# Performance work log

Hardware: AMD Instinct MI355X
Metric: run time of the kernel (lower is better)

## Reference

```python
import jax, jax.numpy as jnp
import numpy as np

H = 11          # hidden size
L = 5           # num layers
G = 4 * H       # gates (i,f,g,o) per PyTorch order


def run_dir(x, Wih, Whh, b, reverse):
    """Single-direction LSTM over x [B,T,D] -> [B,T,H]."""
    pre = jnp.einsum('btd,gd->btg', x, Wih) + b      # [B,T,4H] input projections
    pre = pre.transpose(1, 0, 2)                     # [T,B,4H]
    if reverse:
        pre = pre[::-1]
    B = x.shape[0]
    h0 = jnp.zeros((B, H), x.dtype)
    c0 = jnp.zeros((B, H), x.dtype)

    def step(carry, gt):
        h, c = carry
        g = gt + h @ Whh.T                           # [B,4H]
        i, f, gg, o = jnp.split(g, 4, axis=-1)
        i = jax.nn.sigmoid(i)
        f = jax.nn.sigmoid(f)
        gg = jnp.tanh(gg)
        o = jax.nn.sigmoid(o)
        c = f * c + i * gg
        h = o * jnp.tanh(c)
        return (h, c), h

    _, hs = jax.lax.scan(step, (h0, c0), pre)        # hs [T,B,H]
    if reverse:
        hs = hs[::-1]
    return hs.transpose(1, 0, 2)                     # [B,T,H]


def setup_inputs() -> dict:
    key = jax.random.key(0)
    ks = jax.random.split(key, 6)
    x = jax.random.normal(ks[0], (2048, 1, 32, 512), dtype=jnp.float32)
    # PyTorch LSTM params: layer0 input=1; layers1-4 input=2H (bidir concat)
    W_ih0 = jax.random.normal(ks[1], (2, G, 1), dtype=jnp.float32) * 0.2
    W_ih_rest = jax.random.normal(ks[2], (L - 1, 2, G, 2 * H), dtype=jnp.float32) * 0.1
    W_hh = jax.random.normal(ks[3], (L, 2, G, H), dtype=jnp.float32) * 0.1
    b_ih = jax.random.normal(ks[4], (L, 2, G), dtype=jnp.float32) * 0.05
    b_hh = jax.random.normal(ks[5], (L, 2, G), dtype=jnp.float32) * 0.05
    return {"x": x, "W_ih0": W_ih0, "W_ih_rest": W_ih_rest, "W_hh": W_hh,
            "b_ih": b_ih, "b_hh": b_hh}


def reference(x, W_ih0, W_ih_rest, W_hh, b_ih, b_hh):
    # x: [B, C=1, height, width] -> sum over height -> [B, C, W] -> [B, W, C]
    inp = x.sum(2).transpose(0, 2, 1)                # [B, W, 1]
    for l in range(L):
        outs = []
        for d in range(2):                           # 0=fwd, 1=bwd
            Wih = W_ih0[d] if l == 0 else W_ih_rest[l - 1, d]
            b = b_ih[l, d] + b_hh[l, d]
            outs.append(run_dir(inp, Wih, W_hh[l, d], b, reverse=(d == 1)))
        inp = jnp.concatenate(outs, axis=-1)         # [B, W, 2H]
    return inp
```

## Files before the change

### kernel.cpp

```cpp
#include <hip/hip_runtime.h>

constexpr int TT = 512;
constexpr int BB = 2048;
constexpr int HH = 11;
constexpr int GG = 44;
constexpr int NL = 5;

typedef float v2f __attribute__((ext_vector_type(2)));
typedef float v4f __attribute__((ext_vector_type(4)));

__device__ __forceinline__ float dpp_q0(float v) {
    return __int_as_float(__builtin_amdgcn_mov_dpp(__float_as_int(v), 0x00, 0xF, 0xF, false));
}
__device__ __forceinline__ float dpp_q1(float v) {
    return __int_as_float(__builtin_amdgcn_mov_dpp(__float_as_int(v), 0x55, 0xF, 0xF, false));
}
__device__ __forceinline__ float dpp_q3(float v) {
    return __int_as_float(__builtin_amdgcn_mov_dpp(__float_as_int(v), 0xFF, 0xF, 0xF, false));
}
__device__ __forceinline__ float dpp_qswap2(float v) {
    return __int_as_float(__builtin_amdgcn_mov_dpp(__float_as_int(v), 0x4E, 0xF, 0xF, false));
}

__global__ void reduce_x(const float* __restrict__ x, float* __restrict__ inp) {
    int t = blockIdx.x * 256 + threadIdx.x;
    int b = blockIdx.y;
    const float* p = x + (size_t)b * 32 * TT + t;
    float s = 0.f;
#pragma unroll
    for (int k = 0; k < 32; k++) s += p[k * TT];
    inp[(size_t)b * TT + t] = s;
}

template <int IND>
__global__ __launch_bounds__(256, 4)
void lstm_layer(
    const float* __restrict__ xin,
    float* __restrict__ out,
    const float* __restrict__ Wih,
    const float* __restrict__ Whh,
    const float* __restrict__ bih,
    const float* __restrict__ bhh)
{
    constexpr int NP    = (IND > 1) ? IND / 2 : 1;
    constexpr int CH    = (IND == 1) ? 64 : 32;
    constexpr int NCH   = TT / CH;
    constexpr int NLD   = (CH * IND) / 64;
    constexpr int RS    = (IND == 1) ? 1 : 24;
    constexpr int BUFSZ = CH * RS;

    __shared__ __align__(16) float smem[4 * 2 * BUFSZ];

    const float L2E   = 1.4426950408889634f;
    const float NL2E  = -L2E;
    const float N2L2E = -2.f * L2E;

    int tid  = threadIdx.x;
    int lane = tid & 63;
    int wid  = tid >> 6;
    int u = lane >> 2;
    int q = lane & 3;
    bool active = (u < HH);
    int grow = q * HH + u;

    int seq = __builtin_amdgcn_readfirstlane((int)blockIdx.x * 4 + wid);
    int b = seq >> 1;
    int d = seq & 1;

    float esc    = (q == 2) ? N2L2E : NL2E;
    float ascale = (q == 2) ? 2.f * N2L2E : 1.f;
    float aoff   = (q == 2) ? -N2L2E : 0.f;

    v2f   wih2[NP];
    float wih0 = 0.f;
    v2f   whh2[6];
    v2f   bias2;
    if (active) {
        const float* wi = Wih + (size_t)(d * GG + grow) * IND;
        if constexpr (IND == 1) {
            wih0 = wi[0] * esc;
        } else {
#pragma unroll
            for (int p = 0; p < NP; p++) wih2[p] = ((const v2f*)wi)[p] * esc;
        }
        const float* wh = Whh + (size_t)(d * GG + grow) * HH;
#pragma unroll
        for (int k = 0; k < 5; k++)
            whh2[k] = (v2f){wh[2 * k] * esc, wh[2 * k + 1] * esc};
        whh2[5] = (v2f){wh[10] * esc, 0.f};
        float bv = (bih[d * GG + grow] + bhh[d * GG + grow]) * esc;
        bias2 = (v2f){bv, 0.f};
    } else {
        if constexpr (IND != 1) {
#pragma unroll
            for (int p = 0; p < NP; p++) wih2[p] = (v2f){0.f, 0.f};
        }
#pragma unroll
        for (int k = 0; k < 6; k++) whh2[k] = (v2f){0.f, 0.f};
        bias2 = (v2f){0.f, 0.f};
    }

    float hprev = 0.f;
    float c = 0.f;

    const int ostep = d ? -22 : 22;
    float* op = out + (size_t)b * TT * 22 + (size_t)(d ? (TT - 1) * 22 : 0)
                    + d * HH + u;
    const bool doStore = (q == 0) && active;

    float* xls = smem + wid * (2 * BUFSZ);

    const float* gbase = xin + (size_t)b * TT * IND
                             + (size_t)(d ? (TT - CH) * IND : 0);
    const int gstep = d ? -(CH * IND) : (CH * IND);

    int wdw[NLD];
#pragma unroll
    for (int k = 0; k < NLD; k++) {
        int p = k * 64 + lane;
        int row = p / IND;
        int col = p - row * IND;
        int r2 = d ? (CH - 1 - row) : row;
        wdw[k] = r2 * RS + col;
    }

    {
        float p0[NLD];
#pragma unroll
        for (int k = 0; k < NLD; k++) p0[k] = gbase[k * 64 + lane];
#pragma unroll
        for (int k = 0; k < NLD; k++) xls[wdw[k]] = p0[k];
    }
    int buf = 0;
    const float* lrow = xls;
    const float* gnext = gbase + gstep;

    v2f   xA[NP], xB[NP];
    float xAs = 0.f, xBs = 0.f;

#define LOAD_ROW(DST, PTR)                                                    \
    do {                                                                      \
        if constexpr (IND == 1) {                                             \
            DST##s = (PTR)[0];                                                \
        } else {                                                              \
            _Pragma("unroll")                                                 \
            for (int i4 = 0; i4 < 5; i4++) {                                  \
                v4f t4 = ((const v4f*)(PTR))[i4];                             \
                DST[2 * i4]     = (v2f){t4.x, t4.y};                          \
                DST[2 * i4 + 1] = (v2f){t4.z, t4.w};                          \
            }                                                                 \
            DST[10] = ((const v2f*)(PTR))[10];                                \
        }                                                                     \
    } while (0)

    LOAD_ROW(xA, lrow);

#define LSTM_STEP(XC, XN, DOPF)                                               \
    do {                                                                      \
        v2f accA, accB;                                                       \
        if constexpr (IND == 1) {                                             \
            accA = bias2;                                                     \
            accB = (v2f){0.f, 0.f};                                           \
        } else {                                                              \
            accA = __builtin_elementwise_fma(XC[0], wih2[0], bias2);          \
            accB = XC[1] * wih2[1];                                           \
            _Pragma("unroll")                                                 \
            for (int p = 2; p < NP; p++) {                                    \
                if (p & 1) accB = __builtin_elementwise_fma(XC[p], wih2[p], accB);\
                else       accA = __builtin_elementwise_fma(XC[p], wih2[p], accA);\
            }                                                                 \
        }                                                                     \
        if (DOPF) { lrow += RS; LOAD_ROW(XN, lrow); }                         \
            \
        asm volatile(                                                         \
            "v_readlane_b32 s20, %2, 0\n\t"                                   \
            "v_readlane_b32 s21, %2, 4\n\t"                                   \
            "v_readlane_b32 s22, %2, 8\n\t"                                   \
            "v_readlane_b32 s23, %2, 12\n\t"                                  \
            "v_readlane_b32 s24, %2, 16\n\t"                                  \
            "v_readlane_b32 s25, %2, 20\n\t"                                  \
            "v_readlane_b32 s26, %2, 24\n\t"                                  \
            "v_readlane_b32 s27, %2, 28\n\t"                                  \
            "v_readlane_b32 s28, %2, 32\n\t"                                  \
            "v_readlane_b32 s29, %2, 36\n\t"                                  \
            "v_readlane_b32 s30, %2, 40\n\t"                                  \
            "v_readlane_b32 s31, %2, 44\n\t"                                  \
            "v_pk_fma_f32 %0, s[20:21], %3, %0\n\t"                           \
            "v_pk_fma_f32 %1, s[22:23], %4, %1\n\t"                           \
            "v_pk_fma_f32 %0, s[24:25], %5, %0\n\t"                           \
            "v_pk_fma_f32 %1, s[26:27], %6, %1\n\t"                           \
            "v_pk_fma_f32 %0, s[28:29], %7, %0\n\t"                           \
            "v_pk_fma_f32 %1, s[30:31], %8, %1"                               \
            : "+v"(accA), "+v"(accB)                                          \
            : "v"(hprev), "v"(whh2[0]), "v"(whh2[1]), "v"(whh2[2]),           \
              "v"(whh2[3]), "v"(whh2[4]), "v"(whh2[5])                        \
            : "s20","s21","s22","s23","s24","s25","s26","s27",                \
              "s28","s29","s30","s31");                                       \
        v2f s2 = accA + accB;                                                 \
        float pre = s2.x + s2.y;                                              \
        if constexpr (IND == 1) pre = fmaf(XC##s, wih0, pre);                 \
        float e   = __builtin_amdgcn_exp2f(pre);                              \
        float act = fmaf(ascale, __builtin_amdgcn_rcpf(1.f + e), aoff);       \
        float ig  = act * dpp_qswap2(act);                  \
        float igb = dpp_q0(ig);                                               \
        float fv  = dpp_q1(act);                                              \
        float ov  = dpp_q3(act);                                              \
        c = fmaf(fv, c, igb);                                                 \
        float e2 = __builtin_amdgcn_exp2f(c);                                 \
        float th = fmaf(2.f, __builtin_amdgcn_rcpf(1.f + e2), -1.f);          \
        float h  = ov * th;                                 \
        if (doStore) *op = h;                                                 \
        op += ostep;                                                          \
        hprev = h;                                                            \
    } while (0)

    for (int ch = 0; ch < NCH; ch++) {
        const bool last = (ch + 1 == NCH);
        float pf[NLD];
        if (!last) {
#pragma unroll
            for (int k = 0; k < NLD; k++) pf[k] = gnext[k * 64 + lane];
        }
        for (int sl = 0; sl < CH - 2; sl += 2) {
            LSTM_STEP(xA, xB, true);
            LSTM_STEP(xB, xA, true);
        }
        LSTM_STEP(xA, xB, true);
        LSTM_STEP(xB, xA, false);
        if (!last) {
            float* swn = xls + ((buf ^ 1) ? BUFSZ : 0);
#pragma unroll
            for (int k = 0; k < NLD; k++) swn[wdw[k]] = pf[k];
            buf ^= 1;
            lrow = swn;
            LOAD_ROW(xA, lrow);
            gnext += gstep;
        }
    }
#undef LSTM_STEP
#undef LOAD_ROW
}

extern "C" void kernel_launch(void* const* d_in, const int* in_sizes, int n_in,
                              void* d_out, int out_size, void* d_ws, size_t ws_size,
                              hipStream_t stream) {
    const float* x        = (const float*)d_in[0];
    const float* W_ih0    = (const float*)d_in[1];
    const float* W_ih_rest= (const float*)d_in[2];
    const float* W_hh     = (const float*)d_in[3];
    const float* b_ih     = (const float*)d_in[4];
    const float* b_hh     = (const float*)d_in[5];
    float* out = (float*)d_out;

    const size_t perB = (size_t)TT * 22 * sizeof(float);
    int chunk = BB;
    while (chunk > 2 && (size_t)chunk * perB > ws_size) chunk >>= 1;
    float* wsbuf = (float*)d_ws;

    for (int c0 = 0; c0 < BB; c0 += chunk) {
        const float* xc   = x + (size_t)c0 * 32 * TT;
        float*       outc = out + (size_t)c0 * TT * 22;
        const int nblk = (chunk * 2) / 4;

        reduce_x<<<dim3(2, chunk), 256, 0, stream>>>(xc, wsbuf);

        lstm_layer<1><<<nblk, 256, 0, stream>>>(wsbuf, outc, W_ih0, W_hh, b_ih, b_hh);

        for (int l = 1; l < NL; l++) {
            const float* src = (l & 1) ? outc : wsbuf;
            float*       dst = (l & 1) ? wsbuf : outc;
            lstm_layer<22><<<nblk, 256, 0, stream>>>(
                src, dst,
                W_ih_rest + (size_t)(l - 1) * 2 * GG * 22,
                W_hh + (size_t)l * 2 * GG * HH,
                b_ih + (size_t)l * 2 * GG,
                b_hh + (size_t)l * 2 * GG);
        }
    }
}
```

Measured before the change: 1.230 ms.

## Run forward and backward LSTM directions interleaved in one wavefront

Each wavefront now handles one batch element and runs both directions together, alternating the two independent recurrences step by step. The goal is to hide the latency of the serial dependency chain (readlane, pk_fma, exp, rcp, dpp) by giving the scheduler two independent chains, and to halve the wave count. In exchange it needs more registers (launch bounds lowered to 2 blocks per SM), uses twice the LDS per wave with an unpadded row stride, and has half as many waves resident to hide latency.

```diff
diff --git a/kernel.cpp b/kernel.cpp
--- a/kernel.cpp
+++ b/kernel.cpp
@@ -7,7 +7,6 @@
 constexpr int NL = 5;
 
 typedef float v2f __attribute__((ext_vector_type(2)));
-typedef float v4f __attribute__((ext_vector_type(4)));
 
 __device__ __forceinline__ float dpp_q0(float v) {
     return __int_as_float(__builtin_amdgcn_mov_dpp(__float_as_int(v), 0x00, 0xF, 0xF, false));
@@ -33,7 +32,7 @@
 }
 
 template <int IND>
-__global__ __launch_bounds__(256, 4)
+__global__ __launch_bounds__(256, 2)
 void lstm_layer(
     const float* __restrict__ xin,
     float* __restrict__ out,
@@ -46,10 +45,9 @@
     constexpr int CH    = (IND == 1) ? 64 : 32;
     constexpr int NCH   = TT / CH;
     constexpr int NLD   = (CH * IND) / 64;
-    constexpr int RS    = (IND == 1) ? 1 : 24;
-    constexpr int BUFSZ = CH * RS;
-
-    __shared__ __align__(16) float smem[4 * 2 * BUFSZ];
+    constexpr int BUFSZ = CH * IND;
+
+    __shared__ float smem[4 * 4 * BUFSZ];
 
     const float L2E   = 1.4426950408889634f;
     const float NL2E  = -L2E;
@@ -63,80 +61,96 @@
     bool active = (u < HH);
     int grow = q * HH + u;
 
-    int seq = __builtin_amdgcn_readfirstlane((int)blockIdx.x * 4 + wid);
-    int b = seq >> 1;
-    int d = seq & 1;
+    int b = __builtin_amdgcn_readfirstlane((int)blockIdx.x * 4 + wid);
 
     float esc    = (q == 2) ? N2L2E : NL2E;
     float ascale = (q == 2) ? 2.f * N2L2E : 1.f;
     float aoff   = (q == 2) ? -N2L2E : 0.f;
 
-    v2f   wih2[NP];
-    float wih0 = 0.f;
-    v2f   whh2[6];
-    v2f   bias2;
+    v2f   wihA[NP], wihB[NP];
+    float wihA0 = 0.f, wihB0 = 0.f;
+    v2f   whhA[6], whhB[6];
+    v2f   biasA, biasB;
     if (active) {
-        const float* wi = Wih + (size_t)(d * GG + grow) * IND;
+        const float* wiA = Wih + (size_t)grow * IND;
+        const float* wiB = Wih + (size_t)(GG + grow) * IND;
         if constexpr (IND == 1) {
-            wih0 = wi[0] * esc;
+            wihA0 = wiA[0] * esc;
+            wihB0 = wiB[0] * esc;
         } else {
 #pragma unroll
-            for (int p = 0; p < NP; p++) wih2[p] = ((const v2f*)wi)[p] * esc;
-        }
-        const float* wh = Whh + (size_t)(d * GG + grow) * HH;
-#pragma unroll
-        for (int k = 0; k < 5; k++)
-            whh2[k] = (v2f){wh[2 * k] * esc, wh[2 * k + 1] * esc};
-        whh2[5] = (v2f){wh[10] * esc, 0.f};
-        float bv = (bih[d * GG + grow] + bhh[d * GG + grow]) * esc;
-        bias2 = (v2f){bv, 0.f};
+            for (int p = 0; p < NP; p++) wihA[p] = ((const v2f*)wiA)[p] * esc;
+#pragma unroll
+            for (int p = 0; p < NP; p++) wihB[p] = ((const v2f*)wiB)[p] * esc;
+        }
+        const float* whA = Whh + (size_t)grow * HH;
+        const float* whB = Whh + (size_t)(GG + grow) * HH;
+#pragma unroll
+        for (int k = 0; k < 5; k++) {
+            whhA[k] = (v2f){whA[2 * k] * esc, whA[2 * k + 1] * esc};
+            whhB[k] = (v2f){whB[2 * k] * esc, whB[2 * k + 1] * esc};
+        }
+        whhA[5] = (v2f){whA[10] * esc, 0.f};
+        whhB[5] = (v2f){whB[10] * esc, 0.f};
+        biasA = (v2f){(bih[grow] + bhh[grow]) * esc, 0.f};
+        biasB = (v2f){(bih[GG + grow] + bhh[GG + grow]) * esc, 0.f};
     } else {
         if constexpr (IND != 1) {
 #pragma unroll
-            for (int p = 0; p < NP; p++) wih2[p] = (v2f){0.f, 0.f};
-        }
-#pragma unroll
-        for (int k = 0; k < 6; k++) whh2[k] = (v2f){0.f, 0.f};
-        bias2 = (v2f){0.f, 0.f};
-    }
-
-    float hprev = 0.f;
-    float c = 0.f;
-
-    const int ostep = d ? -22 : 22;
-    float* op = out + (size_t)b * TT * 22 + (size_t)(d ? (TT - 1) * 22 : 0)
-                    + d * HH + u;
+            for (int p = 0; p < NP; p++) { wihA[p] = (v2f){0.f, 0.f}; wihB[p] = (v2f){0.f, 0.f}; }
+        }
+#pragma unroll
+        for (int k = 0; k < 6; k++) { whhA[k] = (v2f){0.f, 0.f}; whhB[k] = (v2f){0.f, 0.f}; }
+        biasA = (v2f){0.f, 0.f};
+        biasB = (v2f){0.f, 0.f};
+    }
+
+    float hA = 0.f, hB = 0.f;
+    float cA = 0.f, cB = 0.f;
+
+    float* opA = out + (size_t)b * TT * 22 + u;
+    float* opB = out + (size_t)b * TT * 22 + (size_t)(TT - 1) * 22 + HH + u;
     const bool doStore = (q == 0) && active;
 
-    float* xls = smem + wid * (2 * BUFSZ);
-
-    const float* gbase = xin + (size_t)b * TT * IND
-                             + (size_t)(d ? (TT - CH) * IND : 0);
-    const int gstep = d ? -(CH * IND) : (CH * IND);
-
-    int wdw[NLD];
+    float* base = smem + wid * (4 * BUFSZ);
+    float* xa0 = base;
+    float* xa1 = base + BUFSZ;
+    float* xb0 = base + 2 * BUFSZ;
+    float* xb1 = base + 3 * BUFSZ;
+
+    const float* gA = xin + (size_t)b * TT * IND;
+    const float* gB = xin + (size_t)b * TT * IND + (size_t)(TT - CH) * IND;
+    const int gstep = CH * IND;
+
+    int wdwB[NLD];
 #pragma unroll
     for (int k = 0; k < NLD; k++) {
         int p = k * 64 + lane;
         int row = p / IND;
         int col = p - row * IND;
-        int r2 = d ? (CH - 1 - row) : row;
-        wdw[k] = r2 * RS + col;
+        wdwB[k] = (CH - 1 - row) * IND + col;
     }
 
     {
-        float p0[NLD];
-#pragma unroll
-        for (int k = 0; k < NLD; k++) p0[k] = gbase[k * 64 + lane];
-#pragma unroll
-        for (int k = 0; k < NLD; k++) xls[wdw[k]] = p0[k];
-    }
-    int buf = 0;
-    const float* lrow = xls;
-    const float* gnext = gbase + gstep;
-
-    v2f   xA[NP], xB[NP];
-    float xAs = 0.f, xBs = 0.f;
+        float pA[NLD], pB[NLD];
+#pragma unroll
+        for (int k = 0; k < NLD; k++) pA[k] = gA[k * 64 + lane];
+#pragma unroll
+        for (int k = 0; k < NLD; k++) pB[k] = gB[k * 64 + lane];
+#pragma unroll
+        for (int k = 0; k < NLD; k++) xa0[k * 64 + lane] = pA[k];
+#pragma unroll
+        for (int k = 0; k < NLD; k++) xb0[wdwB[k]] = pB[k];
+    }
+    const float* gnA = gA + gstep;
+    const float* gnB = gB - gstep;
+    float* bufA = xa0;
+    float* bufB = xb0;
+    const float* lrA = bufA;
+    const float* lrB = bufB;
+
+    v2f   Xa0[NP], Xa1[NP], Xb0r[NP], Xb1r[NP];
+    float Xa0s = 0.f, Xa1s = 0.f, Xb0rs = 0.f, Xb1rs = 0.f;
 
 #define LOAD_ROW(DST, PTR)                                                    \
     do {                                                                      \
@@ -144,100 +158,131 @@
             DST##s = (PTR)[0];                                                \
         } else {                                                              \
             _Pragma("unroll")                                                 \
-            for (int i4 = 0; i4 < 5; i4++) {                                  \
-                v4f t4 = ((const v4f*)(PTR))[i4];                             \
-                DST[2 * i4]     = (v2f){t4.x, t4.y};                          \
-                DST[2 * i4 + 1] = (v2f){t4.z, t4.w};                          \
-            }                                                                 \
-            DST[10] = ((const v2f*)(PTR))[10];                                \
+            for (int p = 0; p < NP; p++) DST[p] = ((const v2f*)(PTR))[p];     \
         }                                                                     \
     } while (0)
 
-    LOAD_ROW(xA, lrow);
-
-#define LSTM_STEP(XC, XN, DOPF)                                               \
+    LOAD_ROW(Xa0, lrA);
+    LOAD_ROW(Xb0r, lrB);
+
+#define HDOT_ASM(A0, A1, HV, W)                                               \
+    asm volatile(                                                             \
+        "v_readlane_b32 s20, %2, 0\n\t"                                       \
+        "v_readlane_b32 s21, %2, 4\n\t"                                       \
+        "v_readlane_b32 s22, %2, 8\n\t"                                       \
+        "v_readlane_b32 s23, %2, 12\n\t"                                      \
+        "v_readlane_b32 s24, %2, 16\n\t"                                      \
+        "v_readlane_b32 s25, %2, 20\n\t"                                      \
+        "v_readlane_b32 s26, %2, 24\n\t"                                      \
+        "v_readlane_b32 s27, %2, 28\n\t"                                      \
+        "v_readlane_b32 s28, %2, 32\n\t"                                      \
+        "v_readlane_b32 s29, %2, 36\n\t"                                      \
+        "v_readlane_b32 s30, %2, 40\n\t"                                      \
+        "v_readlane_b32 s31, %2, 44\n\t"                                      \
+        "v_pk_fma_f32 %0, s[20:21], %3, %0\n\t"                               \
+        "v_pk_fma_f32 %1, s[22:23], %4, %1\n\t"                               \
+        "v_pk_fma_f32 %0, s[24:25], %5, %0\n\t"                               \
+        "v_pk_fma_f32 %1, s[26:27], %6, %1\n\t"                               \
+        "v_pk_fma_f32 %0, s[28:29], %7, %0\n\t"                               \
+        "v_pk_fma_f32 %1, s[30:31], %8, %1"                                   \
+        : "+v"(A0), "+v"(A1)                                                  \
+        : "v"(HV), "v"(W[0]), "v"(W[1]), "v"(W[2]),                           \
+          "v"(W[3]), "v"(W[4]), "v"(W[5])                                     \
+        : "s20","s21","s22","s23","s24","s25","s26","s27",                    \
+          "s28","s29","s30","s31")
+
+#define LSTM_STEP2(CA, NA, CB, NB, DOPF)                                      \
     do {                                                                      \
-        v2f accA, accB;                                                       \
+        v2f aA0, aA1, aB0, aB1;                                               \
         if constexpr (IND == 1) {                                             \
-            accA = bias2;                                                     \
-            accB = (v2f){0.f, 0.f};                                           \
+            aA0 = biasA; aA1 = (v2f){0.f, 0.f};                               \
+            aB0 = biasB; aB1 = (v2f){0.f, 0.f};                               \
         } else {                                                              \
-            accA = __builtin_elementwise_fma(XC[0], wih2[0], bias2);          \
-            accB = XC[1] * wih2[1];                                           \
+            aA0 = __builtin_elementwise_fma(CA[0], wihA[0], biasA);           \
+            aA1 = CA[1] * wihA[1];                                            \
+            aB0 = __builtin_elementwise_fma(CB[0], wihB[0], biasB);           \
+            aB1 = CB[1] * wihB[1];                                            \
             _Pragma("unroll")                                                 \
             for (int p = 2; p < NP; p++) {                                    \
-                if (p & 1) accB = __builtin_elementwise_fma(XC[p], wih2[p], accB);\
-                else       accA = __builtin_elementwise_fma(XC[p], wih2[p], accA);\
+                if (p & 1) { aA1 = __builtin_elementwise_fma(CA[p], wihA[p], aA1); \
+                             aB1 = __builtin_elementwise_fma(CB[p], wihB[p], aB1); } \
+                else       { aA0 = __builtin_elementwise_fma(CA[p], wihA[p], aA0); \
+                             aB0 = __builtin_elementwise_fma(CB[p], wihB[p], aB0); } \
             }                                                                 \
         }                                                                     \
-        if (DOPF) { lrow += RS; LOAD_ROW(XN, lrow); }                         \
-            \
-        asm volatile(                                                         \
-            "v_readlane_b32 s20, %2, 0\n\t"                                   \
-            "v_readlane_b32 s21, %2, 4\n\t"                                   \
-            "v_readlane_b32 s22, %2, 8\n\t"                                   \
-            "v_readlane_b32 s23, %2, 12\n\t"                                  \
-            "v_readlane_b32 s24, %2, 16\n\t"                                  \
-            "v_readlane_b32 s25, %2, 20\n\t"                                  \
-            "v_readlane_b32 s26, %2, 24\n\t"                                  \
-            "v_readlane_b32 s27, %2, 28\n\t"                                  \
-            "v_readlane_b32 s28, %2, 32\n\t"                                  \
-            "v_readlane_b32 s29, %2, 36\n\t"                                  \
-            "v_readlane_b32 s30, %2, 40\n\t"                                  \
-            "v_readlane_b32 s31, %2, 44\n\t"                                  \
-            "v_pk_fma_f32 %0, s[20:21], %3, %0\n\t"                           \
-            "v_pk_fma_f32 %1, s[22:23], %4, %1\n\t"                           \
-            "v_pk_fma_f32 %0, s[24:25], %5, %0\n\t"                           \
-            "v_pk_fma_f32 %1, s[26:27], %6, %1\n\t"                           \
-            "v_pk_fma_f32 %0, s[28:29], %7, %0\n\t"                           \
-            "v_pk_fma_f32 %1, s[30:31], %8, %1"                               \
-            : "+v"(accA), "+v"(accB)                                          \
-            : "v"(hprev), "v"(whh2[0]), "v"(whh2[1]), "v"(whh2[2]),           \
-              "v"(whh2[3]), "v"(whh2[4]), "v"(whh2[5])                        \
-            : "s20","s21","s22","s23","s24","s25","s26","s27",                \
-              "s28","s29","s30","s31");                                       \
-        v2f s2 = accA + accB;                                                 \
-        float pre = s2.x + s2.y;                                              \
-        if constexpr (IND == 1) pre = fmaf(XC##s, wih0, pre);                 \
-        float e   = __builtin_amdgcn_exp2f(pre);                              \
-        float act = fmaf(ascale, __builtin_amdgcn_rcpf(1.f + e), aoff);       \
-        float ig  = act * dpp_qswap2(act);                  \
-        float igb = dpp_q0(ig);                                               \
-        float fv  = dpp_q1(act);                                              \
-        float ov  = dpp_q3(act);                                              \
-        c = fmaf(fv, c, igb);                                                 \
-        float e2 = __builtin_amdgcn_exp2f(c);                                 \
-        float th = fmaf(2.f, __builtin_amdgcn_rcpf(1.f + e2), -1.f);          \
-        float h  = ov * th;                                 \
-        if (doStore) *op = h;                                                 \
-        op += ostep;                                                          \
-        hprev = h;                                                            \
+        if (DOPF) {                                                           \
+            lrA += IND; LOAD_ROW(NA, lrA);                                    \
+            lrB += IND; LOAD_ROW(NB, lrB);                                    \
+        }                                                                     \
+        HDOT_ASM(aA0, aA1, hA, whhA);                                         \
+        HDOT_ASM(aB0, aB1, hB, whhB);                                         \
+        v2f sA = aA0 + aA1;                                                   \
+        v2f sB = aB0 + aB1;                                                   \
+        float preA = sA.x + sA.y;                                             \
+        float preB = sB.x + sB.y;                                             \
+        if constexpr (IND == 1) {                                             \
+            preA = fmaf(CA##s, wihA0, preA);                                  \
+            preB = fmaf(CB##s, wihB0, preB);                                  \
+        }                                                                     \
+        float eA   = __builtin_amdgcn_exp2f(preA);                            \
+        float eB   = __builtin_amdgcn_exp2f(preB);                            \
+        float actA = fmaf(ascale, __builtin_amdgcn_rcpf(1.f + eA), aoff);     \
+        float actB = fmaf(ascale, __builtin_amdgcn_rcpf(1.f + eB), aoff);     \
+        float igA  = actA * dpp_qswap2(actA);                                 \
+        float igB  = actB * dpp_qswap2(actB);                                 \
+        float igbA = dpp_q0(igA);                                             \
+        float igbB = dpp_q0(igB);                                             \
+        float fvA  = dpp_q1(actA);                                            \
+        float fvB  = dpp_q1(actB);                                            \
+        float ovA  = dpp_q3(actA);                                            \
+        float ovB  = dpp_q3(actB);                                            \
+        cA = fmaf(fvA, cA, igbA);                                             \
+        cB = fmaf(fvB, cB, igbB);                                             \
+        float e2A = __builtin_amdgcn_exp2f(cA);                               \
+        float e2B = __builtin_amdgcn_exp2f(cB);                               \
+        float thA = fmaf(2.f, __builtin_amdgcn_rcpf(1.f + e2A), -1.f);        \
+        float thB = fmaf(2.f, __builtin_amdgcn_rcpf(1.f + e2B), -1.f);        \
+        float hA_ = ovA * thA;                                                \
+        float hB_ = ovB * thB;                                                \
+        if (doStore) { *opA = hA_; *opB = hB_; }                              \
+        opA += 22;                                                            \
+        opB -= 22;                                                            \
+        hA = hA_;                                                             \
+        hB = hB_;                                                             \
     } while (0)
 
     for (int ch = 0; ch < NCH; ch++) {
         const bool last = (ch + 1 == NCH);
-        float pf[NLD];
+        float pfA[NLD], pfB[NLD];
         if (!last) {
 #pragma unroll
-            for (int k = 0; k < NLD; k++) pf[k] = gnext[k * 64 + lane];
+            for (int k = 0; k < NLD; k++) pfA[k] = gnA[k * 64 + lane];
+#pragma unroll
+            for (int k = 0; k < NLD; k++) pfB[k] = gnB[k * 64 + lane];
         }
         for (int sl = 0; sl < CH - 2; sl += 2) {
-            LSTM_STEP(xA, xB, true);
-            LSTM_STEP(xB, xA, true);
-        }
-        LSTM_STEP(xA, xB, true);
-        LSTM_STEP(xB, xA, false);
+            LSTM_STEP2(Xa0, Xa1, Xb0r, Xb1r, true);
+            LSTM_STEP2(Xa1, Xa0, Xb1r, Xb0r, true);
+        }
+        LSTM_STEP2(Xa0, Xa1, Xb0r, Xb1r, true);
+        LSTM_STEP2(Xa1, Xa0, Xb1r, Xb0r, false);
         if (!last) {
-            float* swn = xls + ((buf ^ 1) ? BUFSZ : 0);
-#pragma unroll
-            for (int k = 0; k < NLD; k++) swn[wdw[k]] = pf[k];
-            buf ^= 1;
-            lrow = swn;
-            LOAD_ROW(xA, lrow);
-            gnext += gstep;
-        }
-    }
-#undef LSTM_STEP
+            float* nbA = (bufA == xa0) ? xa1 : xa0;
+            float* nbB = (bufB == xb0) ? xb1 : xb0;
+#pragma unroll
+            for (int k = 0; k < NLD; k++) nbA[k * 64 + lane] = pfA[k];
+#pragma unroll
+            for (int k = 0; k < NLD; k++) nbB[wdwB[k]] = pfB[k];
+            bufA = nbA; bufB = nbB;
+            lrA = bufA; lrB = bufB;
+            LOAD_ROW(Xa0, lrA);
+            LOAD_ROW(Xb0r, lrB);
+            gnA += gstep;
+            gnB -= gstep;
+        }
+    }
+#undef LSTM_STEP2
+#undef HDOT_ASM
 #undef LOAD_ROW
 }
 
@@ -254,13 +299,13 @@
 
     const size_t perB = (size_t)TT * 22 * sizeof(float);
     int chunk = BB;
-    while (chunk > 2 && (size_t)chunk * perB > ws_size) chunk >>= 1;
+    while (chunk > 4 && (size_t)chunk * perB > ws_size) chunk >>= 1;
     float* wsbuf = (float*)d_ws;
 
     for (int c0 = 0; c0 < BB; c0 += chunk) {
         const float* xc   = x + (size_t)c0 * 32 * TT;
         float*       outc = out + (size_t)c0 * TT * 22;
-        const int nblk = (chunk * 2) / 4;
+        const int nblk = chunk / 4;
 
         reduce_x<<<dim3(2, chunk), 256, 0, stream>>>(xc, wsbuf);
 
```

Measured after the change: 1.296 ms. 1.05x slower.
